# Performance work log

Hardware: AMD Instinct MI355X
Metric: run time of the kernel (lower is better)

Reference implementation:

```python
import jax, jax.numpy as jnp
import numpy as np

N = 50000
E = 800000
IN_C, HID_C, OUT_C = 128, 128, 40
K = 3  # PyG TAGConv default number of hops


def setup_inputs() -> dict:
    key = jax.random.key(0)
    k1, k2, k3, k4, k5, k6, k7 = jax.random.split(key, 7)
    x = jax.random.normal(k1, (N, IN_C), dtype=jnp.float32)
    edge_index = jax.random.randint(k2, (2, E), 0, N, dtype=jnp.int64)
    # Linear((K+1)*in, out) weights (stored as [in_total, out] for x @ W)
    s1 = 1.0 / np.sqrt((K + 1) * IN_C)
    s2 = 1.0 / np.sqrt((K + 1) * HID_C)
    W1 = jax.random.uniform(k3, ((K + 1) * IN_C, HID_C), jnp.float32, -s1, s1)
    b1 = jax.random.uniform(k4, (HID_C,), jnp.float32, -s1, s1)
    W2 = jax.random.uniform(k5, ((K + 1) * HID_C, OUT_C), jnp.float32, -s2, s2)
    b2 = jax.random.uniform(k6, (OUT_C,), jnp.float32, -s2, s2)
    return {"x": x, "edge_index": edge_index, "W1": W1, "b1": b1, "W2": W2, "b2": b2}


def _sym_norm(src, dst):
    # GCN-style symmetric normalization: deg computed on destination (col)
    deg = jax.ops.segment_sum(jnp.ones((E,), jnp.float32), dst, num_segments=N)
    dis = jnp.where(deg > 0, jax.lax.rsqrt(jnp.maximum(deg, 1.0)), 0.0)
    return dis[src] * dis[dst]  # [E]


def _tag_layer(x, src, dst, norm, W, b):
    xs = [x]
    h = x
    for _ in range(K):
        h = jax.ops.segment_sum(h[src] * norm[:, None], dst, num_segments=N)
        xs.append(h)
    return jnp.concatenate(xs, axis=1) @ W + b


def reference(x, edge_index, W1, b1, W2, b2):
    src, dst = edge_index[0], edge_index[1]
    norm = _sym_norm(src, dst)
    h = jax.nn.relu(_tag_layer(x, src, dst, norm, W1, b1))
    # F.dropout(training=False) is identity at inference
    h = _tag_layer(h, src, dst, norm, W2, b2)
    return jax.nn.log_softmax(h, axis=1)
```

## Files before the change

kernel.cpp:

```cpp
#include <hip/hip_runtime.h>
#include <hip/hip_bf16.h>

#define NNODES 50000
#define NROWP  50176
#define NEDGES 800000
#define KHOP 3
#define SCAN_NB 49
#define NBKT 196
#define BCAP 6144
#define ABLK 400
#define ACH  2000

typedef __attribute__((ext_vector_type(8))) short short8v;
typedef __attribute__((ext_vector_type(8))) __bf16 bf16x8;
typedef __attribute__((ext_vector_type(4))) float f32x4;

__device__ inline unsigned short f2bf(float f) {
  unsigned u = __builtin_bit_cast(unsigned, f);
  u += 0x7fffu + ((u >> 16) & 1u);
  return (unsigned short)(u >> 16);
}
__device__ inline float bflo(unsigned u) { return __builtin_bit_cast(float, u << 16); }
__device__ inline float bfhi(unsigned u) { return __builtin_bit_cast(float, u & 0xffff0000u); }

__device__ inline void gload_lds16(const void* g, void* l) {
  __builtin_amdgcn_global_load_lds(
      (const __attribute__((address_space(1))) unsigned int*)g,
      (__attribute__((address_space(3))) unsigned int*)l, 16, 0, 0);
}

__device__ inline f32x4 mfma_bf16(bf16x8 a, bf16x8 b, f32x4 c) {
  return __builtin_amdgcn_mfma_f32_16x16x32_bf16(a, b, c, 0, 0, 0);
}

__device__ inline void fma8(float* acc, float w, short8v v) {
  uint4 u = __builtin_bit_cast(uint4, v);
  acc[0] = fmaf(w, bflo(u.x), acc[0]);
  acc[1] = fmaf(w, bfhi(u.x), acc[1]);
  acc[2] = fmaf(w, bflo(u.y), acc[2]);
  acc[3] = fmaf(w, bfhi(u.y), acc[3]);
  acc[4] = fmaf(w, bflo(u.z), acc[4]);
  acc[5] = fmaf(w, bfhi(u.z), acc[5]);
  acc[6] = fmaf(w, bflo(u.w), acc[6]);
  acc[7] = fmaf(w, bfhi(u.w), acc[7]);
}

__device__ inline void fma4(float* acc, float w, uint2 v) {
  acc[0] = fmaf(w, bflo(v.x), acc[0]);
  acc[1] = fmaf(w, bfhi(v.x), acc[1]);
  acc[2] = fmaf(w, bflo(v.y), acc[2]);
  acc[3] = fmaf(w, bfhi(v.y), acc[3]);
}

__global__ __launch_bounds__(256) void bucketA_kernel(
    const int* __restrict__ src, const int* __restrict__ dst,
    int* __restrict__ bcur, int2* __restrict__ bkt) {
  __shared__ int2 eb[ACH];
  __shared__ int hist[256];
  __shared__ int base[256];
  int tid = threadIdx.x;
  int e0 = blockIdx.x * ACH;
  int cnt = NEDGES - e0; if (cnt > ACH) cnt = ACH;
  hist[tid] = 0;
  __syncthreads();
  for (int i = tid; i < cnt; i += 256) {
    int s = src[e0 + i], d = dst[e0 + i];
    eb[i] = make_int2(s, d);
    atomicAdd(&hist[d >> 8], 1);
  }
  __syncthreads();
  base[tid] = atomicAdd(&bcur[tid], hist[tid]);
  hist[tid] = 0;
  __syncthreads();
  for (int i = tid; i < cnt; i += 256) {
    int2 e = eb[i];
    int b = e.y >> 8;
    int off = atomicAdd(&hist[b], 1);
    bkt[(size_t)b * BCAP + base[b] + off] = e;
  }
}

__global__ __launch_bounds__(256) void histB_kernel(
    const int* __restrict__ bcur, const int2* __restrict__ bkt,
    int* __restrict__ cnt, int n) {
  __shared__ int h[256];
  int b = blockIdx.x, tid = threadIdx.x;
  h[tid] = 0;
  __syncthreads();
  int sz = bcur[b];
  for (int i = tid; i < sz; i += 256)
    atomicAdd(&h[bkt[(size_t)b * BCAP + i].y & 255], 1);
  __syncthreads();
  int node = b * 256 + tid;
  if (node < n) cnt[node] = h[tid];
}

__global__ __launch_bounds__(256) void bsum_kernel(const int* __restrict__ cnt,
                                                   int* __restrict__ bsums, int n) {
  __shared__ int sd[256];
  int tid = threadIdx.x;
  int base = blockIdx.x * 1024 + tid * 4;
  int s = 0;
  if (base + 4 <= n) {
    int4 v = *(const int4*)&cnt[base];
    s = v.x + v.y + v.z + v.w;
  }
  sd[tid] = s;
  __syncthreads();
  for (int o = 128; o; o >>= 1) {
    if (tid < o) sd[tid] += sd[tid + o];
    __syncthreads();
  }
  if (tid == 0) bsums[blockIdx.x] = sd[0];
}

__global__ __launch_bounds__(64) void bscan_kernel(const int* __restrict__ bsums,
                                                   int* __restrict__ boff,
                                                   int* __restrict__ row_ptr,
                                                   int nb, int n) {
  int tid = threadIdx.x;
  int own = (tid < nb) ? bsums[tid] : 0;
  int v = own;
#pragma unroll
  for (int o = 1; o < 64; o <<= 1) {
    int t = __shfl_up(v, o, 64);
    if (tid >= o) v += t;
  }
  if (tid < nb) boff[tid] = v - own;
  if (tid == 63) row_ptr[n] = v;
}

__global__ __launch_bounds__(256) void bfinal_kernel(const int* __restrict__ cnt,
                                                     const int* __restrict__ boff,
                                                     int* __restrict__ row_ptr,
                                                     float* __restrict__ dis, int n) {
  __shared__ int sd[256];
  int tid = threadIdx.x;
  int base = blockIdx.x * 1024 + tid * 4;
  int4 v = make_int4(0, 0, 0, 0);
  bool ok = (base + 4 <= n);
  if (ok) v = *(const int4*)&cnt[base];
  int s = v.x + v.y + v.z + v.w;
  sd[tid] = s;
  __syncthreads();
  for (int o = 1; o < 256; o <<= 1) {
    int t = (tid >= o) ? sd[tid - o] : 0;
    __syncthreads();
    sd[tid] += t;
    __syncthreads();
  }
  if (ok) {
    int run = boff[blockIdx.x] + sd[tid] - s;
    int4 rp;
    rp.x = run;
    rp.y = run + v.x;
    rp.z = rp.y + v.y;
    rp.w = rp.z + v.z;
    *(int4*)&row_ptr[base] = rp;
    float4 dv;
    dv.x = (v.x > 0) ? rsqrtf((float)v.x) : 0.f;
    dv.y = (v.y > 0) ? rsqrtf((float)v.y) : 0.f;
    dv.z = (v.z > 0) ? rsqrtf((float)v.z) : 0.f;
    dv.w = (v.w > 0) ? rsqrtf((float)v.w) : 0.f;
    *(float4*)&dis[base] = dv;
  }
}

__global__ __launch_bounds__(256) void scatB_kernel(
    const int* __restrict__ bcur, const int2* __restrict__ bkt,
    const int* __restrict__ row_ptr, const float* __restrict__ dis,
    int2* __restrict__ csr, int n) {
  __shared__ int cur[256];
  int b = blockIdx.x, tid = threadIdx.x;
  int node = b * 256 + tid;
  cur[tid] = (node < n) ? row_ptr[node] : 0;
  __syncthreads();
  int sz = bcur[b];
  for (int i = tid; i < sz; i += 256) {
    int2 e = bkt[(size_t)b * BCAP + i];
    int pos = atomicAdd(&cur[e.y & 255], 1);
    int2 ent;
    ent.x = e.x;
    ent.y = __float_as_int(dis[e.x] * dis[e.y]);
    csr[pos] = ent;
  }
}

__global__ void wprep_kernel(const float* __restrict__ W1, const float* __restrict__ W2,
                             unsigned short* __restrict__ W1t,
                             unsigned short* __restrict__ W2pt) {
  int t = blockIdx.x * blockDim.x + threadIdx.x;
  if (t < 512 * 128) {
    int c = t >> 9, k = t & 511;
    W1t[t] = f2bf(W1[(size_t)k * 128 + c]);
  } else if (t < 512 * 128 + 160 * 128) {
    int u = t - 512 * 128;
    int q = u >> 7, r = u & 127;
    int k = q / 40, c = q - k * 40;
    W2pt[u] = f2bf(W2[(size_t)(k * 128 + r) * 40 + c]);
  }
}

__global__ void copyx_kernel(const float* __restrict__ x, unsigned short* __restrict__ P, int n) {
  int t = blockIdx.x * blockDim.x + threadIdx.x;
  int i = t >> 5;
  int c4 = (t & 31) << 2;
  if (i < n) {
    float4 v = *(const float4*)&x[(size_t)i * 128 + c4];
    unsigned lo = (unsigned)f2bf(v.x) | ((unsigned)f2bf(v.y) << 16);
    unsigned hi = (unsigned)f2bf(v.z) | ((unsigned)f2bf(v.w) << 16);
    uint2 o; o.x = lo; o.y = hi;
    *(uint2*)&P[(size_t)i * 512 + c4] = o;
  }
}

__global__ __launch_bounds__(256) void prop128c_kernel(
    const unsigned short* __restrict__ in, unsigned short* __restrict__ out,
    const int* __restrict__ row_ptr, const int2* __restrict__ csr, int n) {
  int node = (int)((blockIdx.x * blockDim.x + threadIdx.x) >> 6);
  int lane = threadIdx.x & 63;
  if (node >= n) return;
  int beg = row_ptr[node], end = row_ptr[node + 1];
  int deg = end - beg;
  int2 ent = make_int2(0, 0);
  if (lane < deg) ent = csr[beg + lane];
  const int grp = lane >> 4, sub = lane & 15;
  float acc[8] = {0.f, 0.f, 0.f, 0.f, 0.f, 0.f, 0.f, 0.f};
  int m = deg < 64 ? deg : 64;
  int j = 0;
  for (; j + 8 <= m; j += 8) {
    int s0 = __shfl(ent.x, j + grp, 64);
    float w0 = __int_as_float(__shfl(ent.y, j + grp, 64));
    int s1 = __shfl(ent.x, j + 4 + grp, 64);
    float w1 = __int_as_float(__shfl(ent.y, j + 4 + grp, 64));
    short8v v0 = *(const short8v*)(in + (size_t)s0 * 512 + sub * 8);
    short8v v1 = *(const short8v*)(in + (size_t)s1 * 512 + sub * 8);
    fma8(acc, w0, v0);
    fma8(acc, w1, v1);
  }
  for (; j < m; j += 4) {
    int idx = j + grp;
    bool act = idx < m;
    int ic = act ? idx : m - 1;
    int s0 = __shfl(ent.x, ic, 64);
    float w0 = __int_as_float(__shfl(ent.y, ic, 64));
    if (!act) w0 = 0.f;
    short8v v0 = *(const short8v*)(in + (size_t)s0 * 512 + sub * 8);
    fma8(acc, w0, v0);
  }
  for (int t = beg + 64; t < end; ++t) {
    int2 e0 = csr[t];
    float w0 = (grp == 0) ? __int_as_float(e0.y) : 0.f;
    short8v v = *(const short8v*)(in + (size_t)e0.x * 512 + sub * 8);
    fma8(acc, w0, v);
  }
#pragma unroll
  for (int i = 0; i < 8; ++i) {
    acc[i] += __shfl_xor(acc[i], 16, 64);
    acc[i] += __shfl_xor(acc[i], 32, 64);
  }
  if (grp == 0) {
    uint4 r;
    r.x = (unsigned)f2bf(acc[0]) | ((unsigned)f2bf(acc[1]) << 16);
    r.y = (unsigned)f2bf(acc[2]) | ((unsigned)f2bf(acc[3]) << 16);
    r.z = (unsigned)f2bf(acc[4]) | ((unsigned)f2bf(acc[5]) << 16);
    r.w = (unsigned)f2bf(acc[6]) | ((unsigned)f2bf(acc[7]) << 16);
    *(uint4*)(out + (size_t)node * 512 + sub * 8) = r;
  }
}

__global__ __launch_bounds__(256) void gemm1m_kernel(
    const unsigned short* __restrict__ A,
    const unsigned short* __restrict__ Bt,
    const float* __restrict__ bias,
    unsigned short* __restrict__ H) {
  __shared__ short As[64 * 32];
  __shared__ short Bs[128 * 32];
  const int tid = threadIdx.x;
  const int lane = tid & 63;
  const int w = tid >> 6;
  const int wr = w & 1;
  const int wc = w >> 1;
  const int row0 = blockIdx.x * 64;
  f32x4 acc[2][4];
#pragma unroll
  for (int i = 0; i < 2; ++i)
#pragma unroll
    for (int j = 0; j < 4; ++j) acc[i][j] = (f32x4)0.f;

  const int lrow = lane >> 2;
  const int lkp = lane & 3;

  for (int k0 = 0; k0 < 512; k0 += 32) {
    gload_lds16(A + (size_t)(row0 + w * 16 + lrow) * 512 + k0 + lkp * 8, &As[w * 512]);
    gload_lds16(Bt + (size_t)(w * 16 + lrow) * 512 + k0 + lkp * 8, &Bs[w * 512]);
    gload_lds16(Bt + (size_t)((w + 4) * 16 + lrow) * 512 + k0 + lkp * 8, &Bs[(w + 4) * 512]);
    __syncthreads();
    const int kg = lane >> 4, rr = lane & 15;
    bf16x8 af[2], bfr[4];
#pragma unroll
    for (int mr = 0; mr < 2; ++mr)
      af[mr] = __builtin_bit_cast(bf16x8,
          *(const short8v*)&As[(wr * 32 + mr * 16 + rr) * 32 + kg * 8]);
#pragma unroll
    for (int nr = 0; nr < 4; ++nr)
      bfr[nr] = __builtin_bit_cast(bf16x8,
          *(const short8v*)&Bs[(wc * 64 + nr * 16 + rr) * 32 + kg * 8]);
#pragma unroll
    for (int mr = 0; mr < 2; ++mr)
#pragma unroll
      for (int nr = 0; nr < 4; ++nr)
        acc[mr][nr] = mfma_bf16(af[mr], bfr[nr], acc[mr][nr]);
    __syncthreads();
  }
  const int cg = lane >> 4, cl = lane & 15;
#pragma unroll
  for (int mr = 0; mr < 2; ++mr)
#pragma unroll
    for (int nr = 0; nr < 4; ++nr) {
      int col = wc * 64 + nr * 16 + cl;
      float bv = bias[col];
#pragma unroll
      for (int j = 0; j < 4; ++j) {
        int row = row0 + wr * 32 + mr * 16 + cg * 4 + j;
        H[(size_t)row * 128 + col] = f2bf(fmaxf(acc[mr][nr][j] + bv, 0.f));
      }
    }
}

__global__ __launch_bounds__(256) void gemm2m_kernel(
    const unsigned short* __restrict__ A,
    const unsigned short* __restrict__ Bt,
    unsigned short* __restrict__ G) {
  __shared__ short As[64 * 32];
  __shared__ short Bs[160 * 32];
  const int tid = threadIdx.x;
  const int lane = tid & 63;
  const int w = tid >> 6;
  const int row0 = blockIdx.x * 64;
  f32x4 acc[10];
#pragma unroll
  for (int i = 0; i < 10; ++i) acc[i] = (f32x4)0.f;
  const int lrow = lane >> 2, lkp = lane & 3;

  for (int k0 = 0; k0 < 128; k0 += 32) {
    gload_lds16(A + (size_t)(row0 + w * 16 + lrow) * 128 + k0 + lkp * 8, &As[w * 512]);
    for (int c = w; c < 10; c += 4)
      gload_lds16(Bt + (size_t)(c * 16 + lrow) * 128 + k0 + lkp * 8, &Bs[c * 512]);
    __syncthreads();
    const int kg = lane >> 4, rr = lane & 15;
    bf16x8 af = __builtin_bit_cast(bf16x8,
        *(const short8v*)&As[(w * 16 + rr) * 32 + kg * 8]);
#pragma unroll
    for (int nr = 0; nr < 10; ++nr) {
      bf16x8 bfr = __builtin_bit_cast(bf16x8,
          *(const short8v*)&Bs[(nr * 16 + rr) * 32 + kg * 8]);
      acc[nr] = mfma_bf16(af, bfr, acc[nr]);
    }
    __syncthreads();
  }
  const int cg = lane >> 4, cl = lane & 15;
#pragma unroll
  for (int nr = 0; nr < 10; ++nr) {
    int col = nr * 16 + cl;
    int k = col / 40;
    int o = col - k * 40;
#pragma unroll
    for (int j = 0; j < 4; ++j) {
      int row = row0 + w * 16 + cg * 4 + j;
      G[(size_t)k * NROWP * 64 + (size_t)row * 64 + o] = f2bf(acc[nr][j]);
    }
  }
}

__global__ __launch_bounds__(256) void prop40c_kernel(
    const unsigned short* __restrict__ in,
    const unsigned short* __restrict__ add,
    unsigned short* __restrict__ out,
    const int* __restrict__ row_ptr, const int2* __restrict__ csr, int n) {
  int node = (int)((blockIdx.x * blockDim.x + threadIdx.x) >> 6);
  int lane = threadIdx.x & 63;
  if (node >= n) return;
  int beg = row_ptr[node], end = row_ptr[node + 1];
  int deg = end - beg;
  int2 ent = make_int2(0, 0);
  if (lane < deg) ent = csr[beg + lane];
  const int grp = lane >> 4, sub = lane & 15;
  float acc[4] = {0.f, 0.f, 0.f, 0.f};
  if (grp == 0) {
    uint2 a = *(const uint2*)(add + (size_t)node * 64 + sub * 4);
    acc[0] = bflo(a.x); acc[1] = bfhi(a.x);
    acc[2] = bflo(a.y); acc[3] = bfhi(a.y);
  }
  int m = deg < 64 ? deg : 64;
  int j = 0;
  for (; j + 8 <= m; j += 8) {
    int s0 = __shfl(ent.x, j + grp, 64);
    float w0 = __int_as_float(__shfl(ent.y, j + grp, 64));
    int s1 = __shfl(ent.x, j + 4 + grp, 64);
    float w1 = __int_as_float(__shfl(ent.y, j + 4 + grp, 64));
    uint2 v0 = *(const uint2*)(in + (size_t)s0 * 64 + sub * 4);
    uint2 v1 = *(const uint2*)(in + (size_t)s1 * 64 + sub * 4);
    fma4(acc, w0, v0);
    fma4(acc, w1, v1);
  }
  for (; j < m; j += 4) {
    int idx = j + grp;
    bool act = idx < m;
    int ic = act ? idx : m - 1;
    int s0 = __shfl(ent.x, ic, 64);
    float w0 = __int_as_float(__shfl(ent.y, ic, 64));
    if (!act) w0 = 0.f;
    uint2 v0 = *(const uint2*)(in + (size_t)s0 * 64 + sub * 4);
    fma4(acc, w0, v0);
  }
  for (int t = beg + 64; t < end; ++t) {
    int2 e0 = csr[t];
    float w = (grp == 0) ? __int_as_float(e0.y) : 0.f;
    uint2 v = *(const uint2*)(in + (size_t)e0.x * 64 + sub * 4);
    fma4(acc, w, v);
  }
#pragma unroll
  for (int i = 0; i < 4; ++i) {
    acc[i] += __shfl_xor(acc[i], 16, 64);
    acc[i] += __shfl_xor(acc[i], 32, 64);
  }
  if (grp == 0) {
    uint2 r;
    r.x = (unsigned)f2bf(acc[0]) | ((unsigned)f2bf(acc[1]) << 16);
    r.y = (unsigned)f2bf(acc[2]) | ((unsigned)f2bf(acc[3]) << 16);
    *(uint2*)(out + (size_t)node * 64 + sub * 4) = r;
  }
}

__global__ __launch_bounds__(256) void prop40c_lsm_kernel(
    const unsigned short* __restrict__ in,
    const unsigned short* __restrict__ add,
    const float* __restrict__ b2,
    float* __restrict__ out,
    const int* __restrict__ row_ptr, const int2* __restrict__ csr, int n) {
  int node = (int)((blockIdx.x * blockDim.x + threadIdx.x) >> 6);
  int lane = threadIdx.x & 63;
  if (node >= n) return;
  int beg = row_ptr[node], end = row_ptr[node + 1];
  int deg = end - beg;
  int2 ent = make_int2(0, 0);
  if (lane < deg) ent = csr[beg + lane];
  const int grp = lane >> 4, sub = lane & 15;
  float acc[4] = {0.f, 0.f, 0.f, 0.f};
  if (grp == 0) {
    uint2 a = *(const uint2*)(add + (size_t)node * 64 + sub * 4);
    acc[0] = bflo(a.x); acc[1] = bfhi(a.x);
    acc[2] = bflo(a.y); acc[3] = bfhi(a.y);
  }
  int m = deg < 64 ? deg : 64;
  int j = 0;
  for (; j + 8 <= m; j += 8) {
    int s0 = __shfl(ent.x, j + grp, 64);
    float w0 = __int_as_float(__shfl(ent.y, j + grp, 64));
    int s1 = __shfl(ent.x, j + 4 + grp, 64);
    float w1 = __int_as_float(__shfl(ent.y, j + 4 + grp, 64));
    uint2 v0 = *(const uint2*)(in + (size_t)s0 * 64 + sub * 4);
    uint2 v1 = *(const uint2*)(in + (size_t)s1 * 64 + sub * 4);
    fma4(acc, w0, v0);
    fma4(acc, w1, v1);
  }
  for (; j < m; j += 4) {
    int idx = j + grp;
    bool act = idx < m;
    int ic = act ? idx : m - 1;
    int s0 = __shfl(ent.x, ic, 64);
    float w0 = __int_as_float(__shfl(ent.y, ic, 64));
    if (!act) w0 = 0.f;
    uint2 v0 = *(const uint2*)(in + (size_t)s0 * 64 + sub * 4);
    fma4(acc, w0, v0);
  }
  for (int t = beg + 64; t < end; ++t) {
    int2 e0 = csr[t];
    float w = (grp == 0) ? __int_as_float(e0.y) : 0.f;
    uint2 v = *(const uint2*)(in + (size_t)e0.x * 64 + sub * 4);
    fma4(acc, w, v);
  }
#pragma unroll
  for (int i = 0; i < 4; ++i) {
    acc[i] += __shfl_xor(acc[i], 16, 64);
    acc[i] += __shfl_xor(acc[i], 32, 64);
  }
  bool val = (sub < 10);
  float vv[4];
  if (val) {
    float4 bv = *(const float4*)(b2 + sub * 4);
    vv[0] = acc[0] + bv.x; vv[1] = acc[1] + bv.y;
    vv[2] = acc[2] + bv.z; vv[3] = acc[3] + bv.w;
  } else {
    vv[0] = vv[1] = vv[2] = vv[3] = -__builtin_inff();
  }
  float mx = fmaxf(fmaxf(vv[0], vv[1]), fmaxf(vv[2], vv[3]));
#pragma unroll
  for (int o = 1; o < 16; o <<= 1) mx = fmaxf(mx, __shfl_xor(mx, o, 64));
  float s = 0.f;
  if (val)
    s = expf(vv[0] - mx) + expf(vv[1] - mx) + expf(vv[2] - mx) + expf(vv[3] - mx);
#pragma unroll
  for (int o = 1; o < 16; o <<= 1) s += __shfl_xor(s, o, 64);
  if (grp == 0 && val) {
    float ls = logf(s);
    float4 o4;
    o4.x = vv[0] - mx - ls; o4.y = vv[1] - mx - ls;
    o4.z = vv[2] - mx - ls; o4.w = vv[3] - mx - ls;
    *(float4*)(out + (size_t)node * 40 + sub * 4) = o4;
  }
}

extern "C" void kernel_launch(void* const* d_in, const int* in_sizes, int n_in,
                              void* d_out, int out_size, void* d_ws, size_t ws_size,
                              hipStream_t stream) {
  const float* x  = (const float*)d_in[0];
  const int*   ei = (const int*)d_in[1];
  const float* W1 = (const float*)d_in[2];
  const float* b1 = (const float*)d_in[3];
  const float* W2 = (const float*)d_in[4];
  const float* b2 = (const float*)d_in[5];
  const int* srcv = ei;
  const int* dstv = ei + NEDGES;
  float* out = (float*)d_out;

  char* wsb = (char*)d_ws;
  size_t off = 0;
  auto alloc = [&](size_t bytes) {
    char* p = wsb + off;
    off += (bytes + 255) & ~(size_t)255;
    return p;
  };
  int*            cnt     = (int*)            alloc((size_t)NNODES * 4);
  float*          dis     = (float*)          alloc((size_t)NNODES * 4);
  int*            row_ptr = (int*)            alloc(((size_t)NNODES + 1) * 4);
  int*            bcur    = (int*)            alloc((size_t)256 * 4);
  int*            bsums   = (int*)            alloc((size_t)SCAN_NB * 4);
  int*            boff    = (int*)            alloc((size_t)SCAN_NB * 4);
  int2*           bkt     = (int2*)           alloc((size_t)NBKT * BCAP * 8);
  int2*           csr     = (int2*)           alloc((size_t)NEDGES * 8);
  unsigned short* W1t     = (unsigned short*) alloc((size_t)128 * 512 * 2);
  unsigned short* W2pt    = (unsigned short*) alloc((size_t)160 * 128 * 2);
  unsigned short* P       = (unsigned short*) alloc((size_t)NROWP * 512 * 2);
  unsigned short* H       = (unsigned short*) alloc((size_t)NROWP * 128 * 2);
  unsigned short* G       = (unsigned short*) alloc((size_t)4 * NROWP * 64 * 2);
  unsigned short* tb      = (unsigned short*) alloc((size_t)NNODES * 64 * 2);
  unsigned short* t2      = (unsigned short*) alloc((size_t)NNODES * 64 * 2);

  unsigned short* G0 = G;
  unsigned short* G1 = G + (size_t)1 * NROWP * 64;
  unsigned short* G2 = G + (size_t)2 * NROWP * 64;
  unsigned short* G3 = G + (size_t)3 * NROWP * 64;

  hipMemsetAsync(bcur, 0, 256 * 4, stream);
  bucketA_kernel<<<ABLK, 256, 0, stream>>>(srcv, dstv, bcur, bkt);
  histB_kernel<<<NBKT, 256, 0, stream>>>(bcur, bkt, cnt, NNODES);
  bsum_kernel<<<SCAN_NB, 256, 0, stream>>>(cnt, bsums, NNODES);
  bscan_kernel<<<1, 64, 0, stream>>>(bsums, boff, row_ptr, SCAN_NB, NNODES);
  bfinal_kernel<<<SCAN_NB, 256, 0, stream>>>(cnt, boff, row_ptr, dis, NNODES);
  scatB_kernel<<<NBKT, 256, 0, stream>>>(bcur, bkt, row_ptr, dis, csr, NNODES);
  wprep_kernel<<<(512 * 128 + 160 * 128 + 255) / 256, 256, 0, stream>>>(W1, W2, W1t, W2pt);
  copyx_kernel<<<((NNODES * 32) + 255) / 256, 256, 0, stream>>>(x, P, NNODES);

  const int prop_blocks = (NNODES * 64 + 255) / 256;
  for (int k = 1; k <= KHOP; ++k)
    prop128c_kernel<<<prop_blocks, 256, 0, stream>>>(P + 128 * (k - 1), P + 128 * k,
                                                     row_ptr, csr, NNODES);
  const int gemm_blocks = (NNODES + 63) / 64;
  gemm1m_kernel<<<gemm_blocks, 256, 0, stream>>>(P, W1t, b1, H);
  gemm2m_kernel<<<gemm_blocks, 256, 0, stream>>>(H, W2pt, G);
  prop40c_kernel<<<prop_blocks, 256, 0, stream>>>(G3, G2, tb, row_ptr, csr, NNODES);
  prop40c_kernel<<<prop_blocks, 256, 0, stream>>>(tb, G1, t2, row_ptr, csr, NNODES);
  prop40c_lsm_kernel<<<prop_blocks, 256, 0, stream>>>(t2, G0, b2, out, row_ptr, csr, NNODES);
}
```

Before: 236.1 us.

## Derive row offsets from bucket counts and unroll gather loops by sixteen

Bucket sizes already give per-bucket edge totals, so a single-block scan over the 196 bucket counts replaces the count/blocksum/scan/finalize chain. Each histogram block then scans its local 256-node counts and writes row_ptr and dis directly, which removes two kernel launches and the intermediate cnt array. The gather loops in the 128-wide and 40-wide propagation kernels also gain a 16-neighbor unrolled stage, so four independent row loads are in flight per group. That raises register pressure in exchange for more memory-level parallelism.

```diff
diff --git a/kernel.cpp b/kernel.cpp
--- a/kernel.cpp
+++ b/kernel.cpp
@@ -5,7 +5,6 @@
 #define NROWP  50176
 #define NEDGES 800000
 #define KHOP 3
-#define SCAN_NB 49
 #define NBKT 196
 #define BCAP 6144
 #define ABLK 400
@@ -80,10 +79,29 @@
   }
 }
 
-__global__ __launch_bounds__(256) void histB_kernel(
+__global__ __launch_bounds__(256) void bktscan_kernel(
+    const int* __restrict__ bcur, int* __restrict__ boff, int* __restrict__ row_ptr) {
+  __shared__ int sd[256];
+  int tid = threadIdx.x;
+  int own = (tid < NBKT) ? bcur[tid] : 0;
+  sd[tid] = own;
+  __syncthreads();
+  for (int o = 1; o < 256; o <<= 1) {
+    int t = (tid >= o) ? sd[tid - o] : 0;
+    __syncthreads();
+    sd[tid] += t;
+    __syncthreads();
+  }
+  if (tid < NBKT) boff[tid] = sd[tid] - own;
+  if (tid == 255) row_ptr[NNODES] = sd[255];
+}
+
+__global__ __launch_bounds__(256) void histC_kernel(
     const int* __restrict__ bcur, const int2* __restrict__ bkt,
-    int* __restrict__ cnt, int n) {
+    const int* __restrict__ boff, int* __restrict__ row_ptr,
+    float* __restrict__ dis, int n) {
   __shared__ int h[256];
+  __shared__ int sc[256];
   int b = blockIdx.x, tid = threadIdx.x;
   h[tid] = 0;
   __syncthreads();
@@ -91,78 +109,19 @@
   for (int i = tid; i < sz; i += 256)
     atomicAdd(&h[bkt[(size_t)b * BCAP + i].y & 255], 1);
   __syncthreads();
+  int own = h[tid];
+  sc[tid] = own;
+  __syncthreads();
+  for (int o = 1; o < 256; o <<= 1) {
+    int t = (tid >= o) ? sc[tid - o] : 0;
+    __syncthreads();
+    sc[tid] += t;
+    __syncthreads();
+  }
   int node = b * 256 + tid;
-  if (node < n) cnt[node] = h[tid];
-}
-
-__global__ __launch_bounds__(256) void bsum_kernel(const int* __restrict__ cnt,
-                                                   int* __restrict__ bsums, int n) {
-  __shared__ int sd[256];
-  int tid = threadIdx.x;
-  int base = blockIdx.x * 1024 + tid * 4;
-  int s = 0;
-  if (base + 4 <= n) {
-    int4 v = *(const int4*)&cnt[base];
-    s = v.x + v.y + v.z + v.w;
-  }
-  sd[tid] = s;
-  __syncthreads();
-  for (int o = 128; o; o >>= 1) {
-    if (tid < o) sd[tid] += sd[tid + o];
-    __syncthreads();
-  }
-  if (tid == 0) bsums[blockIdx.x] = sd[0];
-}
-
-__global__ __launch_bounds__(64) void bscan_kernel(const int* __restrict__ bsums,
-                                                   int* __restrict__ boff,
-                                                   int* __restrict__ row_ptr,
-                                                   int nb, int n) {
-  int tid = threadIdx.x;
-  int own = (tid < nb) ? bsums[tid] : 0;
-  int v = own;
-#pragma unroll
-  for (int o = 1; o < 64; o <<= 1) {
-    int t = __shfl_up(v, o, 64);
-    if (tid >= o) v += t;
-  }
-  if (tid < nb) boff[tid] = v - own;
-  if (tid == 63) row_ptr[n] = v;
-}
-
-__global__ __launch_bounds__(256) void bfinal_kernel(const int* __restrict__ cnt,
-                                                     const int* __restrict__ boff,
-                                                     int* __restrict__ row_ptr,
-                                                     float* __restrict__ dis, int n) {
-  __shared__ int sd[256];
-  int tid = threadIdx.x;
-  int base = blockIdx.x * 1024 + tid * 4;
-  int4 v = make_int4(0, 0, 0, 0);
-  bool ok = (base + 4 <= n);
-  if (ok) v = *(const int4*)&cnt[base];
-  int s = v.x + v.y + v.z + v.w;
-  sd[tid] = s;
-  __syncthreads();
-  for (int o = 1; o < 256; o <<= 1) {
-    int t = (tid >= o) ? sd[tid - o] : 0;
-    __syncthreads();
-    sd[tid] += t;
-    __syncthreads();
-  }
-  if (ok) {
-    int run = boff[blockIdx.x] + sd[tid] - s;
-    int4 rp;
-    rp.x = run;
-    rp.y = run + v.x;
-    rp.z = rp.y + v.y;
-    rp.w = rp.z + v.z;
-    *(int4*)&row_ptr[base] = rp;
-    float4 dv;
-    dv.x = (v.x > 0) ? rsqrtf((float)v.x) : 0.f;
-    dv.y = (v.y > 0) ? rsqrtf((float)v.y) : 0.f;
-    dv.z = (v.z > 0) ? rsqrtf((float)v.z) : 0.f;
-    dv.w = (v.w > 0) ? rsqrtf((float)v.w) : 0.f;
-    *(float4*)&dis[base] = dv;
+  if (node < n) {
+    row_ptr[node] = boff[b] + sc[tid] - own;
+    dis[node] = (own > 0) ? rsqrtf((float)own) : 0.f;
   }
 }
 
@@ -228,6 +187,24 @@
   float acc[8] = {0.f, 0.f, 0.f, 0.f, 0.f, 0.f, 0.f, 0.f};
   int m = deg < 64 ? deg : 64;
   int j = 0;
+  for (; j + 16 <= m; j += 16) {
+    int s0 = __shfl(ent.x, j + grp, 64);
+    float w0 = __int_as_float(__shfl(ent.y, j + grp, 64));
+    int s1 = __shfl(ent.x, j + 4 + grp, 64);
+    float w1 = __int_as_float(__shfl(ent.y, j + 4 + grp, 64));
+    int s2 = __shfl(ent.x, j + 8 + grp, 64);
+    float w2 = __int_as_float(__shfl(ent.y, j + 8 + grp, 64));
+    int s3 = __shfl(ent.x, j + 12 + grp, 64);
+    float w3 = __int_as_float(__shfl(ent.y, j + 12 + grp, 64));
+    short8v v0 = *(const short8v*)(in + (size_t)s0 * 512 + sub * 8);
+    short8v v1 = *(const short8v*)(in + (size_t)s1 * 512 + sub * 8);
+    short8v v2 = *(const short8v*)(in + (size_t)s2 * 512 + sub * 8);
+    short8v v3 = *(const short8v*)(in + (size_t)s3 * 512 + sub * 8);
+    fma8(acc, w0, v0);
+    fma8(acc, w1, v1);
+    fma8(acc, w2, v2);
+    fma8(acc, w3, v3);
+  }
   for (; j + 8 <= m; j += 8) {
     int s0 = __shfl(ent.x, j + grp, 64);
     float w0 = __int_as_float(__shfl(ent.y, j + grp, 64));
@@ -394,6 +371,24 @@
   }
   int m = deg < 64 ? deg : 64;
   int j = 0;
+  for (; j + 16 <= m; j += 16) {
+    int s0 = __shfl(ent.x, j + grp, 64);
+    float w0 = __int_as_float(__shfl(ent.y, j + grp, 64));
+    int s1 = __shfl(ent.x, j + 4 + grp, 64);
+    float w1 = __int_as_float(__shfl(ent.y, j + 4 + grp, 64));
+    int s2 = __shfl(ent.x, j + 8 + grp, 64);
+    float w2 = __int_as_float(__shfl(ent.y, j + 8 + grp, 64));
+    int s3 = __shfl(ent.x, j + 12 + grp, 64);
+    float w3 = __int_as_float(__shfl(ent.y, j + 12 + grp, 64));
+    uint2 v0 = *(const uint2*)(in + (size_t)s0 * 64 + sub * 4);
+    uint2 v1 = *(const uint2*)(in + (size_t)s1 * 64 + sub * 4);
+    uint2 v2 = *(const uint2*)(in + (size_t)s2 * 64 + sub * 4);
+    uint2 v3 = *(const uint2*)(in + (size_t)s3 * 64 + sub * 4);
+    fma4(acc, w0, v0);
+    fma4(acc, w1, v1);
+    fma4(acc, w2, v2);
+    fma4(acc, w3, v3);
+  }
   for (; j + 8 <= m; j += 8) {
     int s0 = __shfl(ent.x, j + grp, 64);
     float w0 = __int_as_float(__shfl(ent.y, j + grp, 64));
@@ -455,6 +450,24 @@
   }
   int m = deg < 64 ? deg : 64;
   int j = 0;
+  for (; j + 16 <= m; j += 16) {
+    int s0 = __shfl(ent.x, j + grp, 64);
+    float w0 = __int_as_float(__shfl(ent.y, j + grp, 64));
+    int s1 = __shfl(ent.x, j + 4 + grp, 64);
+    float w1 = __int_as_float(__shfl(ent.y, j + 4 + grp, 64));
+    int s2 = __shfl(ent.x, j + 8 + grp, 64);
+    float w2 = __int_as_float(__shfl(ent.y, j + 8 + grp, 64));
+    int s3 = __shfl(ent.x, j + 12 + grp, 64);
+    float w3 = __int_as_float(__shfl(ent.y, j + 12 + grp, 64));
+    uint2 v0 = *(const uint2*)(in + (size_t)s0 * 64 + sub * 4);
+    uint2 v1 = *(const uint2*)(in + (size_t)s1 * 64 + sub * 4);
+    uint2 v2 = *(const uint2*)(in + (size_t)s2 * 64 + sub * 4);
+    uint2 v3 = *(const uint2*)(in + (size_t)s3 * 64 + sub * 4);
+    fma4(acc, w0, v0);
+    fma4(acc, w1, v1);
+    fma4(acc, w2, v2);
+    fma4(acc, w3, v3);
+  }
   for (; j + 8 <= m; j += 8) {
     int s0 = __shfl(ent.x, j + grp, 64);
     float w0 = __int_as_float(__shfl(ent.y, j + grp, 64));
@@ -532,12 +545,10 @@
     off += (bytes + 255) & ~(size_t)255;
     return p;
   };
-  int*            cnt     = (int*)            alloc((size_t)NNODES * 4);
   float*          dis     = (float*)          alloc((size_t)NNODES * 4);
   int*            row_ptr = (int*)            alloc(((size_t)NNODES + 1) * 4);
   int*            bcur    = (int*)            alloc((size_t)256 * 4);
-  int*            bsums   = (int*)            alloc((size_t)SCAN_NB * 4);
-  int*            boff    = (int*)            alloc((size_t)SCAN_NB * 4);
+  int*            boff    = (int*)            alloc((size_t)NBKT * 4);
   int2*           bkt     = (int2*)           alloc((size_t)NBKT * BCAP * 8);
   int2*           csr     = (int2*)           alloc((size_t)NEDGES * 8);
   unsigned short* W1t     = (unsigned short*) alloc((size_t)128 * 512 * 2);
@@ -555,10 +566,8 @@
 
   hipMemsetAsync(bcur, 0, 256 * 4, stream);
   bucketA_kernel<<<ABLK, 256, 0, stream>>>(srcv, dstv, bcur, bkt);
-  histB_kernel<<<NBKT, 256, 0, stream>>>(bcur, bkt, cnt, NNODES);
-  bsum_kernel<<<SCAN_NB, 256, 0, stream>>>(cnt, bsums, NNODES);
-  bscan_kernel<<<1, 64, 0, stream>>>(bsums, boff, row_ptr, SCAN_NB, NNODES);
-  bfinal_kernel<<<SCAN_NB, 256, 0, stream>>>(cnt, boff, row_ptr, dis, NNODES);
+  bktscan_kernel<<<1, 256, 0, stream>>>(bcur, boff, row_ptr);
+  histC_kernel<<<NBKT, 256, 0, stream>>>(bcur, bkt, boff, row_ptr, dis, NNODES);
   scatB_kernel<<<NBKT, 256, 0, stream>>>(bcur, bkt, row_ptr, dis, csr, NNODES);
   wprep_kernel<<<(512 * 128 + 160 * 128 + 255) / 256, 256, 0, stream>>>(W1, W2, W1t, W2pt);
   copyx_kernel<<<((NNODES * 32) + 255) / 256, 256, 0, stream>>>(x, P, NNODES);
```

New measurement: 229.9 us. 1.03x faster.
